# Kernel optimization log

Measured on AMD Instinct MI355X. Metric: run time of the kernel, lower is better.

## Reference

```python
import jax, jax.numpy as jnp
import numpy as np

B, N, D = 2, 2048, 768
H = 12
HD = D // H  # 64

def setup_inputs() -> dict:
    key = jax.random.key(0)
    ks = jax.random.split(key, 5)
    scale = 1.0 / np.sqrt(D)
    return {
        "x": jax.random.normal(ks[0], (B, N, D), dtype=jnp.float32),
        "W_kqv": jax.random.normal(ks[1], (H, 3 * HD, D), dtype=jnp.float32) * scale,
        "b_kqv": jax.random.normal(ks[2], (H, 3 * HD), dtype=jnp.float32) * 0.01,
        "W_proj": jax.random.normal(ks[3], (D, D), dtype=jnp.float32) * scale,
        "b_proj": jax.random.normal(ks[4], (D,), dtype=jnp.float32) * 0.01,
    }

def reference(x, W_kqv, b_kqv, W_proj, b_proj):
    # Per-head Linear: x @ W_h^T + b_h, all heads at once -> [B, H, N, 3*HD]
    kqv = jnp.einsum('bnd,hod->bhno', x, W_kqv) + b_kqv[None, :, None, :]
    k, q, v = jnp.split(kqv, 3, axis=-1)  # each [B, H, N, HD]
    # scores = q @ k^T / sqrt(head_dim)  (attention_scores(a=k, b=q))
    scores = jnp.einsum('bhqd,bhkd->bhqk', q, k) / jnp.sqrt(jnp.asarray(HD, x.dtype))
    # causal mask (tril): masked_fill with -inf where mask == 0
    causal = jnp.tril(jnp.ones((N, N), dtype=bool))
    scores = jnp.where(causal[None, None, :, :], scores, -jnp.inf)
    attn = jax.nn.softmax(scores, axis=-1)
    sa = jnp.einsum('bhqk,bhkd->bhqd', attn, v)  # [B, H, N, HD]
    # concat heads along feature dim (head order preserved)
    sa = sa.transpose(0, 2, 1, 3).reshape(B, N, D)
    # output projection
    return sa @ W_proj.T + b_proj
```

## Files before the change

### kernel.cpp

```cpp
#include <hip/hip_runtime.h>

#define BB 2
#define SEQ 2048
#define DIM 768
#define NH 12
#define HD 64

typedef _Float16 half8 __attribute__((ext_vector_type(8)));
typedef float floatx4 __attribute__((ext_vector_type(4)));

__device__ __forceinline__ void gl_lds16(const _Float16* g, _Float16* l) {
    __builtin_amdgcn_global_load_lds(
        (const __attribute__((address_space(1))) void*)g,
        (__attribute__((address_space(3))) void*)l, 16, 0, 0);
}

__global__ __launch_bounds__(256)
void cvt3(const float* __restrict__ s0, _Float16* __restrict__ d0, int nb0,
          const float* __restrict__ s1, _Float16* __restrict__ d1, int nb1,
          const float* __restrict__ s2, _Float16* __restrict__ d2) {
    int b = blockIdx.x;
    const float* s; _Float16* d;
    if (b < nb0)            { s = s0; d = d0; }
    else if (b < nb0 + nb1) { s = s1; d = d1; b -= nb0; }
    else                    { s = s2; d = d2; b -= nb0 + nb1; }
    const int i = (b * 256 + threadIdx.x) * 8;
    float4 a = *(const float4*)(s + i);
    float4 c = *(const float4*)(s + i + 4);
    half8 h;
    h[0] = (_Float16)a.x; h[1] = (_Float16)a.y; h[2] = (_Float16)a.z; h[3] = (_Float16)a.w;
    h[4] = (_Float16)c.x; h[5] = (_Float16)c.y; h[6] = (_Float16)c.z; h[7] = (_Float16)c.w;
    *(half8*)(d + i) = h;
}

#define GEMM_CORE(ATYPE_PTR, BTYPE_PTR)                                         \
    __shared__ _Float16 Asl[128 * 32];                                          \
    __shared__ _Float16 Bsl[128 * 32];                                          \
    const int t = threadIdx.x, w = t >> 6, lane = t & 63;                       \
    const int quad = lane >> 4, l15 = lane & 15;                                \
    const int wm = w >> 1, wn = w & 1;                                          \
    const int m0 = blockIdx.y * 128, c0 = blockIdx.x * 128;                     \
    const floatx4 z4 = {0.f, 0.f, 0.f, 0.f};                                    \
    floatx4 acc[4][4];                                                          \
    _Pragma("unroll") for (int i = 0; i < 4; ++i)                               \
        _Pragma("unroll") for (int j = 0; j < 4; ++j) acc[i][j] = z4;           \
    const _Float16* pA = ATYPE_PTR + (size_t)(m0 + w * 32 + l15) * DIM + quad * 8; \
    const _Float16* pB = BTYPE_PTR + (size_t)(c0 + w * 32 + l15) * DIM + quad * 8; \
    _Float16* ldsA0 = &Asl[(w * 2 + 0) * 512];                                  \
    _Float16* ldsA1 = &Asl[(w * 2 + 1) * 512];                                  \
    _Float16* ldsB0 = &Bsl[(w * 2 + 0) * 512];                                  \
    _Float16* ldsB1 = &Bsl[(w * 2 + 1) * 512];                                  \
    for (int k0 = 0; k0 < DIM; k0 += 32) {                                      \
        __syncthreads();                                                        \
        gl_lds16(pA + k0, ldsA0);                                               \
        gl_lds16(pA + k0 + 16 * DIM, ldsA1);                                    \
        gl_lds16(pB + k0, ldsB0);                                               \
        gl_lds16(pB + k0 + 16 * DIM, ldsB1);                                    \
        __syncthreads();                                                        \
        half8 af[4], bf[4];                                                     \
        _Pragma("unroll") for (int i = 0; i < 4; ++i)                           \
            af[i] = *(const half8*)&Asl[(wm * 4 + i) * 512 + lane * 8];         \
        _Pragma("unroll") for (int j = 0; j < 4; ++j)                           \
            bf[j] = *(const half8*)&Bsl[(wn * 4 + j) * 512 + lane * 8];         \
        _Pragma("unroll") for (int i = 0; i < 4; ++i)                           \
            _Pragma("unroll") for (int j = 0; j < 4; ++j)                       \
                acc[i][j] = __builtin_amdgcn_mfma_f32_16x16x32_f16(             \
                    af[i], bf[j], acc[i][j], 0, 0, 0);                          \
    }

__global__ __launch_bounds__(256)
void kqv_gemm2(const _Float16* __restrict__ xh, const _Float16* __restrict__ Wh,
               const float* __restrict__ bias, _Float16* __restrict__ kb,
               _Float16* __restrict__ qb, _Float16* __restrict__ vb) {
    GEMM_CORE(xh, Wh)
    #pragma unroll
    for (int j = 0; j < 4; ++j) {
        const int cbase = c0 + (wn * 4 + j) * 16;
        const int h = cbase / 192;
        const int rem = cbase - h * 192;
        const int part = rem >> 6;
        const int d = (rem & 63) + l15;
        _Float16* dst = (part == 0) ? kb : (part == 1 ? qb : vb);
        const float bv = bias[cbase + l15];
        #pragma unroll
        for (int i = 0; i < 4; ++i)
            #pragma unroll
            for (int r = 0; r < 4; ++r) {
                const int m = m0 + (wm * 4 + i) * 16 + quad * 4 + r;
                const int bidx = m >> 11, n = m & (SEQ - 1);
                dst[(((size_t)(bidx * NH + h) * SEQ + n) << 6) + d] =
                    (_Float16)(acc[i][j][r] + bv);
            }
    }
}

__global__ __launch_bounds__(256)
void proj_gemm2(const _Float16* __restrict__ A, const _Float16* __restrict__ Wh,
                const float* __restrict__ bias, float* __restrict__ out) {
    GEMM_CORE(A, Wh)
    #pragma unroll
    for (int j = 0; j < 4; ++j) {
        const int cbase = c0 + (wn * 4 + j) * 16;
        const float bv = bias[cbase + l15];
        #pragma unroll
        for (int i = 0; i < 4; ++i)
            #pragma unroll
            for (int r = 0; r < 4; ++r) {
                const int m = m0 + (wm * 4 + i) * 16 + quad * 4 + r;
                out[(size_t)m * DIM + cbase + l15] = acc[i][j][r] + bv;
            }
    }
}

__global__ __launch_bounds__(256)
void v_transpose(const _Float16* __restrict__ vb, _Float16* __restrict__ vbT) {
    __shared__ _Float16 T[64 * 72];
    const int t = threadIdx.x;
    const int s0 = blockIdx.x * 64;
    const size_t base = (size_t)blockIdx.y * (SEQ * HD);
    {
        const int s = t >> 2, doff = (t & 3) * 16;
        const _Float16* src = vb + base + (size_t)(s0 + s) * HD + doff;
        *(half8*)&T[s * 72 + doff]     = *(const half8*)src;
        *(half8*)&T[s * 72 + doff + 8] = *(const half8*)(src + 8);
    }
    __syncthreads();
    {
        const int d = t >> 2, soff = (t & 3) * 16;
        half8 o0, o1;
        #pragma unroll
        for (int k = 0; k < 8; ++k) o0[k] = T[(soff + k) * 72 + d];
        #pragma unroll
        for (int k = 0; k < 8; ++k) o1[k] = T[(soff + 8 + k) * 72 + d];
        _Float16* dst = vbT + base + (size_t)d * SEQ + s0 + soff;
        *(half8*)dst       = o0;
        *(half8*)(dst + 8) = o1;
    }
}

__global__ __launch_bounds__(256)
void attn_mfma(const _Float16* __restrict__ qb, const _Float16* __restrict__ kbuf,
               const _Float16* __restrict__ vbT, _Float16* __restrict__ sa) {
    __shared__ _Float16 Kl[2][64 * 64];
    __shared__ _Float16 Vl[2][64 * 64];
    __shared__ _Float16 Pl[4][16 * 72];
    const int qt = blockIdx.x, bh = blockIdx.y;
    const int t = threadIdx.x, w = t >> 6, lane = t & 63, quad = lane >> 4, l15 = lane & 15;
    const size_t base = (size_t)bh * (SEQ * HD);
    const int i0 = qt * 64 + w * 16;
    _Float16* Pw = Pl[w];
    const _Float16* Kg = kbuf + base;
    const _Float16* Vg = vbT + base;

    const int lr = lane >> 3, gg = lane & 7;
    const int gs = (gg ^ (lr & 7)) * 8;

    half8 aq[2];
    aq[0] = *(const half8*)(qb + base + (size_t)(i0 + l15) * HD + quad * 8);
    aq[1] = *(const half8*)(qb + base + (size_t)(i0 + l15) * HD + 32 + quad * 8);
    #pragma unroll
    for (int k = 0; k < 8; ++k) {
        aq[0][k] = aq[0][k] * (_Float16)0.125f;
        aq[1][k] = aq[1][k] * (_Float16)0.125f;
    }

    const floatx4 z4 = {0.f, 0.f, 0.f, 0.f};
    floatx4 O[4];
    #pragma unroll
    for (int dt = 0; dt < 4; ++dt) O[dt] = z4;
    float l_part[4] = {0.f, 0.f, 0.f, 0.f};

    #pragma unroll
    for (int p = 0; p < 2; ++p) {
        const int c = w * 2 + p, row = c * 8 + lr;
        gl_lds16(Kg + (size_t)row * HD + gs,  &Kl[0][c * 512]);
        gl_lds16(Vg + (size_t)row * SEQ + gs, &Vl[0][c * 512]);
    }

    const int swz = l15 & 7;

    for (int kt = 0; kt <= qt; ++kt) {
        const int buf = kt & 1;
        const int j0 = kt * 64;
        __syncthreads();

        if (kt < qt) {
            const _Float16* Kn = Kg + (size_t)(j0 + 64) * HD;
            const _Float16* Vn = Vg + (j0 + 64);
            #pragma unroll
            for (int p = 0; p < 2; ++p) {
                const int c = w * 2 + p, row = c * 8 + lr;
                gl_lds16(Kn + (size_t)row * HD + gs,  &Kl[buf ^ 1][c * 512]);
                gl_lds16(Vn + (size_t)row * SEQ + gs, &Vl[buf ^ 1][c * 512]);
            }
        }

        floatx4 S[4];
        #pragma unroll
        for (int nt = 0; nt < 4; ++nt) S[nt] = z4;
        #pragma unroll
        for (int ks = 0; ks < 2; ++ks)
            #pragma unroll
            for (int nt = 0; nt < 4; ++nt) {
                half8 bk = *(const half8*)&Kl[buf][(nt * 16 + l15) * 64 +
                                                   (((ks * 4 + quad) ^ swz) << 3)];
                S[nt] = __builtin_amdgcn_mfma_f32_16x16x32_f16(aq[ks], bk, S[nt], 0, 0, 0);
            }

        const bool diag = (kt == qt);
        asm volatile("" ::: "memory");
        #pragma unroll
        for (int nt = 0; nt < 4; ++nt) {
            const int j = j0 + nt * 16 + l15;
            #pragma unroll
            for (int r = 0; r < 4; ++r) {
                float p = __expf(S[nt][r]);
                if (diag && j > (i0 + quad * 4 + r)) p = 0.f;
                l_part[r] += p;
                Pw[(quad * 4 + r) * 72 + nt * 16 + l15] = (_Float16)p;
            }
        }
        asm volatile("" ::: "memory");
        #pragma unroll
        for (int ks = 0; ks < 2; ++ks) {
            half8 ap = *(const half8*)&Pw[l15 * 72 + ks * 32 + quad * 8];
            #pragma unroll
            for (int dt = 0; dt < 4; ++dt) {
                half8 bv = *(const half8*)&Vl[buf][(dt * 16 + l15) * 64 +
                                                    (((ks * 4 + quad) ^ swz) << 3)];
                O[dt] = __builtin_amdgcn_mfma_f32_16x16x32_f16(ap, bv, O[dt], 0, 0, 0);
            }
        }
    }

    const int bidx = bh / NH, h = bh - bidx * NH;
    #pragma unroll
    for (int r = 0; r < 4; ++r) {
        float rs = l_part[r];
        #pragma unroll
        for (int off = 1; off < 16; off <<= 1) rs += __shfl_xor(rs, off);
        const float inv = 1.0f / rs;
        const int i = i0 + quad * 4 + r;
        #pragma unroll
        for (int dt = 0; dt < 4; ++dt)
            sa[(size_t)(bidx * SEQ + i) * DIM + h * HD + dt * 16 + l15] =
                (_Float16)(O[dt][r] * inv);
    }
}

extern "C" void kernel_launch(void* const* d_in, const int* in_sizes, int n_in,
                              void* d_out, int out_size, void* d_ws, size_t ws_size,
                              hipStream_t stream) {
    (void)in_sizes; (void)n_in; (void)out_size; (void)ws_size;
    const float* x  = (const float*)d_in[0];
    const float* Wk = (const float*)d_in[1];
    const float* bk = (const float*)d_in[2];
    const float* Wp = (const float*)d_in[3];
    const float* bp = (const float*)d_in[4];
    float* out = (float*)d_out;

    _Float16* ws = (_Float16*)d_ws;
    const size_t per = (size_t)BB * NH * SEQ * HD;
    const int nx = BB * SEQ * DIM;
    const int nwk = NH * 3 * HD * DIM;
    const int nwp = DIM * DIM;
    _Float16* kb  = ws;
    _Float16* qb  = ws + per;
    _Float16* vb  = ws + 2 * per;
    _Float16* vbT = ws + 3 * per;
    _Float16* sa  = ws + 4 * per;
    _Float16* xh  = ws + 5 * per;
    _Float16* Wkh = xh + nx;
    _Float16* Wph = Wkh + nwk;

    const int nb0 = nx / 2048, nb1 = nwk / 2048, nb2 = nwp / 2048;
    cvt3<<<dim3(nb0 + nb1 + nb2), 256, 0, stream>>>(x, xh, nb0, Wk, Wkh, nb1, Wp, Wph);

    kqv_gemm2 <<<dim3(18, 32), 256, 0, stream>>>(xh, Wkh, bk, kb, qb, vb);
    v_transpose<<<dim3(32, 24), 256, 0, stream>>>(vb, vbT);
    attn_mfma <<<dim3(32, 24), 256, 0, stream>>>(qb, kb, vbT, sa);
    proj_gemm2<<<dim3(6, 32), 256, 0, stream>>>(sa, Wph, bp, out);
}
```

Baseline: 191.3 us.

## Double-buffer GEMM LDS tiles and widen attention query tile to 128 rows

The shared GEMM core now double-buffers its A/B tiles in LDS and prefetches the next K-slice before computing the current one, which removes one barrier per iteration and overlaps global loads with MFMA work. The attention kernel now gives each block 128 query rows (32 per wave, two row tiles), so every K/V tile loaded into LDS serves twice as many rows. Blocks are launched in reverse order so the longest causal blocks start first. In exchange there are half as many attention blocks (384), more registers per wave, waves that skip tiles fully above the diagonal while still joining the barriers, and more LDS use.

Result: slower. 215.2 us (+12.5%).

```diff
diff --git a/kernel.cpp b/kernel.cpp
--- a/kernel.cpp
+++ b/kernel.cpp
@@ -33,9 +33,9 @@
     *(half8*)(d + i) = h;
 }
 
-#define GEMM_CORE(ATYPE_PTR, BTYPE_PTR)                                         \
-    __shared__ _Float16 Asl[128 * 32];                                          \
-    __shared__ _Float16 Bsl[128 * 32];                                          \
+#define GEMM_CORE(APTR, BPTR)                                                   \
+    __shared__ _Float16 Asl[2][128 * 32];                                       \
+    __shared__ _Float16 Bsl[2][128 * 32];                                       \
     const int t = threadIdx.x, w = t >> 6, lane = t & 63;                       \
     const int quad = lane >> 4, l15 = lane & 15;                                \
     const int wm = w >> 1, wn = w & 1;                                          \
@@ -44,24 +44,26 @@
     floatx4 acc[4][4];                                                          \
     _Pragma("unroll") for (int i = 0; i < 4; ++i)                               \
         _Pragma("unroll") for (int j = 0; j < 4; ++j) acc[i][j] = z4;           \
-    const _Float16* pA = ATYPE_PTR + (size_t)(m0 + w * 32 + l15) * DIM + quad * 8; \
-    const _Float16* pB = BTYPE_PTR + (size_t)(c0 + w * 32 + l15) * DIM + quad * 8; \
-    _Float16* ldsA0 = &Asl[(w * 2 + 0) * 512];                                  \
-    _Float16* ldsA1 = &Asl[(w * 2 + 1) * 512];                                  \
-    _Float16* ldsB0 = &Bsl[(w * 2 + 0) * 512];                                  \
-    _Float16* ldsB1 = &Bsl[(w * 2 + 1) * 512];                                  \
-    for (int k0 = 0; k0 < DIM; k0 += 32) {                                      \
+    const _Float16* pA = APTR + (size_t)(m0 + w * 32 + l15) * DIM + quad * 8;   \
+    const _Float16* pB = BPTR + (size_t)(c0 + w * 32 + l15) * DIM + quad * 8;   \
+    gl_lds16(pA,            &Asl[0][(w * 2 + 0) * 512]);                        \
+    gl_lds16(pA + 16 * DIM, &Asl[0][(w * 2 + 1) * 512]);                        \
+    gl_lds16(pB,            &Bsl[0][(w * 2 + 0) * 512]);                        \
+    gl_lds16(pB + 16 * DIM, &Bsl[0][(w * 2 + 1) * 512]);                        \
+    for (int k0 = 0, it = 0; k0 < DIM; k0 += 32, ++it) {                        \
+        const int buf = it & 1;                                                 \
         __syncthreads();                                                        \
-        gl_lds16(pA + k0, ldsA0);                                               \
-        gl_lds16(pA + k0 + 16 * DIM, ldsA1);                                    \
-        gl_lds16(pB + k0, ldsB0);                                               \
-        gl_lds16(pB + k0 + 16 * DIM, ldsB1);                                    \
-        __syncthreads();                                                        \
+        if (k0 + 32 < DIM) {                                                    \
+            gl_lds16(pA + k0 + 32,            &Asl[buf ^ 1][(w * 2 + 0) * 512]);\
+            gl_lds16(pA + k0 + 32 + 16 * DIM, &Asl[buf ^ 1][(w * 2 + 1) * 512]);\
+            gl_lds16(pB + k0 + 32,            &Bsl[buf ^ 1][(w * 2 + 0) * 512]);\
+            gl_lds16(pB + k0 + 32 + 16 * DIM, &Bsl[buf ^ 1][(w * 2 + 1) * 512]);\
+        }                                                                       \
         half8 af[4], bf[4];                                                     \
         _Pragma("unroll") for (int i = 0; i < 4; ++i)                           \
-            af[i] = *(const half8*)&Asl[(wm * 4 + i) * 512 + lane * 8];         \
+            af[i] = *(const half8*)&Asl[buf][(wm * 4 + i) * 512 + lane * 8];    \
         _Pragma("unroll") for (int j = 0; j < 4; ++j)                           \
-            bf[j] = *(const half8*)&Bsl[(wn * 4 + j) * 512 + lane * 8];         \
+            bf[j] = *(const half8*)&Bsl[buf][(wn * 4 + j) * 512 + lane * 8];    \
         _Pragma("unroll") for (int i = 0; i < 4; ++i)                           \
             _Pragma("unroll") for (int j = 0; j < 4; ++j)                       \
                 acc[i][j] = __builtin_amdgcn_mfma_f32_16x16x32_f16(             \
@@ -143,32 +145,38 @@
                const _Float16* __restrict__ vbT, _Float16* __restrict__ sa) {
     __shared__ _Float16 Kl[2][64 * 64];
     __shared__ _Float16 Vl[2][64 * 64];
-    __shared__ _Float16 Pl[4][16 * 72];
-    const int qt = blockIdx.x, bh = blockIdx.y;
+    __shared__ _Float16 Pl[4][2][16 * 72];
+    const int Q = 15 - blockIdx.x;
+    const int bh = blockIdx.y;
     const int t = threadIdx.x, w = t >> 6, lane = t & 63, quad = lane >> 4, l15 = lane & 15;
     const size_t base = (size_t)bh * (SEQ * HD);
-    const int i0 = qt * 64 + w * 16;
-    _Float16* Pw = Pl[w];
+    const int i0 = Q * 128 + w * 32;
     const _Float16* Kg = kbuf + base;
     const _Float16* Vg = vbT + base;
+    const int nkt = 2 * Q + 2;
 
     const int lr = lane >> 3, gg = lane & 7;
     const int gs = (gg ^ (lr & 7)) * 8;
 
-    half8 aq[2];
-    aq[0] = *(const half8*)(qb + base + (size_t)(i0 + l15) * HD + quad * 8);
-    aq[1] = *(const half8*)(qb + base + (size_t)(i0 + l15) * HD + 32 + quad * 8);
-    #pragma unroll
-    for (int k = 0; k < 8; ++k) {
-        aq[0][k] = aq[0][k] * (_Float16)0.125f;
-        aq[1][k] = aq[1][k] * (_Float16)0.125f;
-    }
+    half8 aq[2][2];
+    #pragma unroll
+    for (int rt = 0; rt < 2; ++rt)
+        #pragma unroll
+        for (int ks = 0; ks < 2; ++ks) {
+            aq[rt][ks] = *(const half8*)(qb + base +
+                          (size_t)(i0 + rt * 16 + l15) * HD + ks * 32 + quad * 8);
+            #pragma unroll
+            for (int k = 0; k < 8; ++k)
+                aq[rt][ks][k] = aq[rt][ks][k] * (_Float16)0.125f;
+        }
 
     const floatx4 z4 = {0.f, 0.f, 0.f, 0.f};
-    floatx4 O[4];
-    #pragma unroll
-    for (int dt = 0; dt < 4; ++dt) O[dt] = z4;
-    float l_part[4] = {0.f, 0.f, 0.f, 0.f};
+    floatx4 O[2][4];
+    float l_part[2][4];
+    #pragma unroll
+    for (int rt = 0; rt < 2; ++rt)
+        #pragma unroll
+        for (int k = 0; k < 4; ++k) { O[rt][k] = z4; l_part[rt][k] = 0.f; }
 
     #pragma unroll
     for (int p = 0; p < 2; ++p) {
@@ -179,12 +187,12 @@
 
     const int swz = l15 & 7;
 
-    for (int kt = 0; kt <= qt; ++kt) {
+    for (int kt = 0; kt < nkt; ++kt) {
         const int buf = kt & 1;
         const int j0 = kt * 64;
         __syncthreads();
 
-        if (kt < qt) {
+        if (kt + 1 < nkt) {
             const _Float16* Kn = Kg + (size_t)(j0 + 64) * HD;
             const _Float16* Vn = Vg + (j0 + 64);
             #pragma unroll
@@ -194,58 +202,68 @@
                 gl_lds16(Vn + (size_t)row * SEQ + gs, &Vl[buf ^ 1][c * 512]);
             }
         }
-
-        floatx4 S[4];
-        #pragma unroll
-        for (int nt = 0; nt < 4; ++nt) S[nt] = z4;
+        if (j0 > i0 + 31) continue;
+
+        floatx4 S[2][4];
+        #pragma unroll
+        for (int rt = 0; rt < 2; ++rt)
+            #pragma unroll
+            for (int nt = 0; nt < 4; ++nt) S[rt][nt] = z4;
         #pragma unroll
         for (int ks = 0; ks < 2; ++ks)
             #pragma unroll
             for (int nt = 0; nt < 4; ++nt) {
                 half8 bk = *(const half8*)&Kl[buf][(nt * 16 + l15) * 64 +
                                                    (((ks * 4 + quad) ^ swz) << 3)];
-                S[nt] = __builtin_amdgcn_mfma_f32_16x16x32_f16(aq[ks], bk, S[nt], 0, 0, 0);
-            }
-
-        const bool diag = (kt == qt);
+                S[0][nt] = __builtin_amdgcn_mfma_f32_16x16x32_f16(aq[0][ks], bk, S[0][nt], 0, 0, 0);
+                S[1][nt] = __builtin_amdgcn_mfma_f32_16x16x32_f16(aq[1][ks], bk, S[1][nt], 0, 0, 0);
+            }
+
+        const bool needmask = (j0 + 63 > i0);
         asm volatile("" ::: "memory");
         #pragma unroll
-        for (int nt = 0; nt < 4; ++nt) {
-            const int j = j0 + nt * 16 + l15;
-            #pragma unroll
-            for (int r = 0; r < 4; ++r) {
-                float p = __expf(S[nt][r]);
-                if (diag && j > (i0 + quad * 4 + r)) p = 0.f;
-                l_part[r] += p;
-                Pw[(quad * 4 + r) * 72 + nt * 16 + l15] = (_Float16)p;
-            }
-        }
+        for (int rt = 0; rt < 2; ++rt)
+            #pragma unroll
+            for (int nt = 0; nt < 4; ++nt) {
+                const int j = j0 + nt * 16 + l15;
+                #pragma unroll
+                for (int r = 0; r < 4; ++r) {
+                    float p = __expf(S[rt][nt][r]);
+                    if (needmask && j > (i0 + rt * 16 + quad * 4 + r)) p = 0.f;
+                    l_part[rt][r] += p;
+                    Pl[w][rt][(quad * 4 + r) * 72 + nt * 16 + l15] = (_Float16)p;
+                }
+            }
         asm volatile("" ::: "memory");
         #pragma unroll
         for (int ks = 0; ks < 2; ++ks) {
-            half8 ap = *(const half8*)&Pw[l15 * 72 + ks * 32 + quad * 8];
+            half8 ap0 = *(const half8*)&Pl[w][0][l15 * 72 + ks * 32 + quad * 8];
+            half8 ap1 = *(const half8*)&Pl[w][1][l15 * 72 + ks * 32 + quad * 8];
             #pragma unroll
             for (int dt = 0; dt < 4; ++dt) {
                 half8 bv = *(const half8*)&Vl[buf][(dt * 16 + l15) * 64 +
                                                     (((ks * 4 + quad) ^ swz) << 3)];
-                O[dt] = __builtin_amdgcn_mfma_f32_16x16x32_f16(ap, bv, O[dt], 0, 0, 0);
+                O[0][dt] = __builtin_amdgcn_mfma_f32_16x16x32_f16(ap0, bv, O[0][dt], 0, 0, 0);
+                O[1][dt] = __builtin_amdgcn_mfma_f32_16x16x32_f16(ap1, bv, O[1][dt], 0, 0, 0);
             }
         }
     }
 
     const int bidx = bh / NH, h = bh - bidx * NH;
     #pragma unroll
-    for (int r = 0; r < 4; ++r) {
-        float rs = l_part[r];
-        #pragma unroll
-        for (int off = 1; off < 16; off <<= 1) rs += __shfl_xor(rs, off);
-        const float inv = 1.0f / rs;
-        const int i = i0 + quad * 4 + r;
-        #pragma unroll
-        for (int dt = 0; dt < 4; ++dt)
-            sa[(size_t)(bidx * SEQ + i) * DIM + h * HD + dt * 16 + l15] =
-                (_Float16)(O[dt][r] * inv);
-    }
+    for (int rt = 0; rt < 2; ++rt)
+        #pragma unroll
+        for (int r = 0; r < 4; ++r) {
+            float rs = l_part[rt][r];
+            #pragma unroll
+            for (int off = 1; off < 16; off <<= 1) rs += __shfl_xor(rs, off);
+            const float inv = 1.0f / rs;
+            const int i = i0 + rt * 16 + quad * 4 + r;
+            #pragma unroll
+            for (int dt = 0; dt < 4; ++dt)
+                sa[(size_t)(bidx * SEQ + i) * DIM + h * HD + dt * 16 + l15] =
+                    (_Float16)(O[rt][dt][r] * inv);
+        }
 }
 
 extern "C" void kernel_launch(void* const* d_in, const int* in_sizes, int n_in,
@@ -263,7 +281,6 @@
     const size_t per = (size_t)BB * NH * SEQ * HD;
     const int nx = BB * SEQ * DIM;
     const int nwk = NH * 3 * HD * DIM;
-    const int nwp = DIM * DIM;
     _Float16* kb  = ws;
     _Float16* qb  = ws + per;
     _Float16* vb  = ws + 2 * per;
@@ -273,11 +290,11 @@
     _Float16* Wkh = xh + nx;
     _Float16* Wph = Wkh + nwk;
 
-    const int nb0 = nx / 2048, nb1 = nwk / 2048, nb2 = nwp / 2048;
+    const int nb0 = nx / 2048, nb1 = nwk / 2048, nb2 = (DIM * DIM) / 2048;
     cvt3<<<dim3(nb0 + nb1 + nb2), 256, 0, stream>>>(x, xh, nb0, Wk, Wkh, nb1, Wp, Wph);
 
     kqv_gemm2 <<<dim3(18, 32), 256, 0, stream>>>(xh, Wkh, bk, kb, qb, vb);
     v_transpose<<<dim3(32, 24), 256, 0, stream>>>(vb, vbT);
-    attn_mfma <<<dim3(32, 24), 256, 0, stream>>>(qb, kb, vbT, sa);
+    attn_mfma <<<dim3(16, 24), 256, 0, stream>>>(qb, kb, vbT, sa);
     proj_gemm2<<<dim3(6, 32), 256, 0, stream>>>(sa, Wph, bp, out);
 }
```

## Split causal attention KV range across blocks and double-buffer GEMM LDS tiles

Applied to the files above, without the earlier changes.

Attention query tiles with long causal KV ranges are now split into up to four chunks of eight KV tiles, each handled by its own block. Partial unnormalized outputs and row sums go to workspace, and a new combine kernel sums them and normalizes. This removes the load imbalance where late query tiles dominate runtime, at the cost of an extra launch and extra global traffic for the partials. Separately, the shared GEMM core now double-buffers its LDS tiles so the next K slice loads while the current one is computed, and drops one barrier per iteration.

Result: no change. 188.9 us (-1.2%).

```diff
diff --git a/kernel.cpp b/kernel.cpp
--- a/kernel.cpp
+++ b/kernel.cpp
@@ -33,9 +33,9 @@
     *(half8*)(d + i) = h;
 }
 
-#define GEMM_CORE(ATYPE_PTR, BTYPE_PTR)                                         \
-    __shared__ _Float16 Asl[128 * 32];                                          \
-    __shared__ _Float16 Bsl[128 * 32];                                          \
+#define GEMM_CORE(APTR, BPTR)                                                   \
+    __shared__ _Float16 Asl[2][128 * 32];                                       \
+    __shared__ _Float16 Bsl[2][128 * 32];                                       \
     const int t = threadIdx.x, w = t >> 6, lane = t & 63;                       \
     const int quad = lane >> 4, l15 = lane & 15;                                \
     const int wm = w >> 1, wn = w & 1;                                          \
@@ -44,24 +44,26 @@
     floatx4 acc[4][4];                                                          \
     _Pragma("unroll") for (int i = 0; i < 4; ++i)                               \
         _Pragma("unroll") for (int j = 0; j < 4; ++j) acc[i][j] = z4;           \
-    const _Float16* pA = ATYPE_PTR + (size_t)(m0 + w * 32 + l15) * DIM + quad * 8; \
-    const _Float16* pB = BTYPE_PTR + (size_t)(c0 + w * 32 + l15) * DIM + quad * 8; \
-    _Float16* ldsA0 = &Asl[(w * 2 + 0) * 512];                                  \
-    _Float16* ldsA1 = &Asl[(w * 2 + 1) * 512];                                  \
-    _Float16* ldsB0 = &Bsl[(w * 2 + 0) * 512];                                  \
-    _Float16* ldsB1 = &Bsl[(w * 2 + 1) * 512];                                  \
-    for (int k0 = 0; k0 < DIM; k0 += 32) {                                      \
+    const _Float16* pA = APTR + (size_t)(m0 + w * 32 + l15) * DIM + quad * 8;   \
+    const _Float16* pB = BPTR + (size_t)(c0 + w * 32 + l15) * DIM + quad * 8;   \
+    gl_lds16(pA,            &Asl[0][(w * 2 + 0) * 512]);                        \
+    gl_lds16(pA + 16 * DIM, &Asl[0][(w * 2 + 1) * 512]);                        \
+    gl_lds16(pB,            &Bsl[0][(w * 2 + 0) * 512]);                        \
+    gl_lds16(pB + 16 * DIM, &Bsl[0][(w * 2 + 1) * 512]);                        \
+    for (int k0 = 0, it = 0; k0 < DIM; k0 += 32, ++it) {                        \
+        const int buf = it & 1;                                                 \
         __syncthreads();                                                        \
-        gl_lds16(pA + k0, ldsA0);                                               \
-        gl_lds16(pA + k0 + 16 * DIM, ldsA1);                                    \
-        gl_lds16(pB + k0, ldsB0);                                               \
-        gl_lds16(pB + k0 + 16 * DIM, ldsB1);                                    \
-        __syncthreads();                                                        \
+        if (k0 + 32 < DIM) {                                                    \
+            gl_lds16(pA + k0 + 32,            &Asl[buf ^ 1][(w * 2 + 0) * 512]);\
+            gl_lds16(pA + k0 + 32 + 16 * DIM, &Asl[buf ^ 1][(w * 2 + 1) * 512]);\
+            gl_lds16(pB + k0 + 32,            &Bsl[buf ^ 1][(w * 2 + 0) * 512]);\
+            gl_lds16(pB + k0 + 32 + 16 * DIM, &Bsl[buf ^ 1][(w * 2 + 1) * 512]);\
+        }                                                                       \
         half8 af[4], bf[4];                                                     \
         _Pragma("unroll") for (int i = 0; i < 4; ++i)                           \
-            af[i] = *(const half8*)&Asl[(wm * 4 + i) * 512 + lane * 8];         \
+            af[i] = *(const half8*)&Asl[buf][(wm * 4 + i) * 512 + lane * 8];    \
         _Pragma("unroll") for (int j = 0; j < 4; ++j)                           \
-            bf[j] = *(const half8*)&Bsl[(wn * 4 + j) * 512 + lane * 8];         \
+            bf[j] = *(const half8*)&Bsl[buf][(wn * 4 + j) * 512 + lane * 8];    \
         _Pragma("unroll") for (int i = 0; i < 4; ++i)                           \
             _Pragma("unroll") for (int j = 0; j < 4; ++j)                       \
                 acc[i][j] = __builtin_amdgcn_mfma_f32_16x16x32_f16(             \
@@ -140,11 +142,20 @@
 
 __global__ __launch_bounds__(256)
 void attn_mfma(const _Float16* __restrict__ qb, const _Float16* __restrict__ kbuf,
-               const _Float16* __restrict__ vbT, _Float16* __restrict__ sa) {
+               const _Float16* __restrict__ vbT, _Float16* __restrict__ sa,
+               _Float16* __restrict__ Opart, float* __restrict__ lpart) {
     __shared__ _Float16 Kl[2][64 * 64];
     __shared__ _Float16 Vl[2][64 * 64];
     __shared__ _Float16 Pl[4][16 * 72];
-    const int qt = blockIdx.x, bh = blockIdx.y;
+    int u = blockIdx.x, qt, p, np;
+    if (u < 8)       { qt = u;                            p = 0;      np = 1; }
+    else if (u < 24) { int v = u - 8;  qt = 8  + (v >> 1); p = v & 1; np = 2; }
+    else if (u < 48) { int v = u - 24; qt = 16 + v / 3;    p = v % 3; np = 3; }
+    else             { int v = u - 48; qt = 24 + (v >> 2); p = v & 3; np = 4; }
+    const int kt0 = p * 8;
+    const int ktn = (p == np - 1) ? (qt - kt0 + 1) : 8;
+
+    const int bh = blockIdx.y;
     const int t = threadIdx.x, w = t >> 6, lane = t & 63, quad = lane >> 4, l15 = lane & 15;
     const size_t base = (size_t)bh * (SEQ * HD);
     const int i0 = qt * 64 + w * 16;
@@ -171,25 +182,26 @@
     float l_part[4] = {0.f, 0.f, 0.f, 0.f};
 
     #pragma unroll
-    for (int p = 0; p < 2; ++p) {
-        const int c = w * 2 + p, row = c * 8 + lr;
-        gl_lds16(Kg + (size_t)row * HD + gs,  &Kl[0][c * 512]);
-        gl_lds16(Vg + (size_t)row * SEQ + gs, &Vl[0][c * 512]);
+    for (int pp = 0; pp < 2; ++pp) {
+        const int c = w * 2 + pp, row = c * 8 + lr;
+        gl_lds16(Kg + (size_t)(kt0 * 64 + row) * HD + gs,  &Kl[0][c * 512]);
+        gl_lds16(Vg + (size_t)row * SEQ + kt0 * 64 + gs,   &Vl[0][c * 512]);
     }
 
     const int swz = l15 & 7;
 
-    for (int kt = 0; kt <= qt; ++kt) {
-        const int buf = kt & 1;
+    for (int it = 0; it < ktn; ++it) {
+        const int kt = kt0 + it;
+        const int buf = it & 1;
         const int j0 = kt * 64;
         __syncthreads();
 
-        if (kt < qt) {
+        if (it + 1 < ktn) {
             const _Float16* Kn = Kg + (size_t)(j0 + 64) * HD;
             const _Float16* Vn = Vg + (j0 + 64);
             #pragma unroll
-            for (int p = 0; p < 2; ++p) {
-                const int c = w * 2 + p, row = c * 8 + lr;
+            for (int pp = 0; pp < 2; ++pp) {
+                const int c = w * 2 + pp, row = c * 8 + lr;
                 gl_lds16(Kn + (size_t)row * HD + gs,  &Kl[buf ^ 1][c * 512]);
                 gl_lds16(Vn + (size_t)row * SEQ + gs, &Vl[buf ^ 1][c * 512]);
             }
@@ -214,10 +226,10 @@
             const int j = j0 + nt * 16 + l15;
             #pragma unroll
             for (int r = 0; r < 4; ++r) {
-                float p = __expf(S[nt][r]);
-                if (diag && j > (i0 + quad * 4 + r)) p = 0.f;
-                l_part[r] += p;
-                Pw[(quad * 4 + r) * 72 + nt * 16 + l15] = (_Float16)p;
+                float pv = __expf(S[nt][r]);
+                if (diag && j > (i0 + quad * 4 + r)) pv = 0.f;
+                l_part[r] += pv;
+                Pw[(quad * 4 + r) * 72 + nt * 16 + l15] = (_Float16)pv;
             }
         }
         asm volatile("" ::: "memory");
@@ -233,19 +245,69 @@
         }
     }
 
+    if (np == 1) {
+        const int bidx = bh / NH, h = bh - bidx * NH;
+        #pragma unroll
+        for (int r = 0; r < 4; ++r) {
+            float rs = l_part[r];
+            #pragma unroll
+            for (int off = 1; off < 16; off <<= 1) rs += __shfl_xor(rs, off);
+            const float inv = 1.0f / rs;
+            const int i = i0 + quad * 4 + r;
+            #pragma unroll
+            for (int dt = 0; dt < 4; ++dt)
+                sa[(size_t)(bidx * SEQ + i) * DIM + h * HD + dt * 16 + l15] =
+                    (_Float16)(O[dt][r] * inv);
+        }
+    } else {
+        const size_t slot = ((size_t)(bh * 32 + qt) * 4 + p);
+        _Float16* Od = Opart + slot * 4096;
+        float*    ld = lpart + slot * 64;
+        #pragma unroll
+        for (int r = 0; r < 4; ++r) {
+            float rs = l_part[r];
+            #pragma unroll
+            for (int off = 1; off < 16; off <<= 1) rs += __shfl_xor(rs, off);
+            const int row = w * 16 + quad * 4 + r;
+            ld[row] = rs;
+            #pragma unroll
+            for (int dt = 0; dt < 4; ++dt)
+                Od[row * 64 + dt * 16 + l15] = (_Float16)O[dt][r];
+        }
+    }
+}
+
+__global__ __launch_bounds__(256)
+void attn_combine(const _Float16* __restrict__ Opart, const float* __restrict__ lpart,
+                  _Float16* __restrict__ sa) {
+    const int qt = 8 + blockIdx.x;
+    const int bh = blockIdx.y;
+    const int np = (qt >> 3) + 1;
+    const int t = threadIdx.x;
+    const int row = t >> 2, d0 = (t & 3) * 16;
+    const size_t slot0 = ((size_t)(bh * 32 + qt) * 4);
+
+    float lsum = 0.f;
+    for (int p = 0; p < np; ++p) lsum += lpart[(slot0 + p) * 64 + row];
+
+    float acc[16];
+    #pragma unroll
+    for (int k = 0; k < 16; ++k) acc[k] = 0.f;
+    for (int p = 0; p < np; ++p) {
+        const _Float16* src = Opart + (slot0 + p) * 4096 + row * 64 + d0;
+        half8 a = *(const half8*)src;
+        half8 b = *(const half8*)(src + 8);
+        #pragma unroll
+        for (int k = 0; k < 8; ++k) { acc[k] += (float)a[k]; acc[8 + k] += (float)b[k]; }
+    }
+    const float inv = 1.0f / lsum;
     const int bidx = bh / NH, h = bh - bidx * NH;
-    #pragma unroll
-    for (int r = 0; r < 4; ++r) {
-        float rs = l_part[r];
-        #pragma unroll
-        for (int off = 1; off < 16; off <<= 1) rs += __shfl_xor(rs, off);
-        const float inv = 1.0f / rs;
-        const int i = i0 + quad * 4 + r;
-        #pragma unroll
-        for (int dt = 0; dt < 4; ++dt)
-            sa[(size_t)(bidx * SEQ + i) * DIM + h * HD + dt * 16 + l15] =
-                (_Float16)(O[dt][r] * inv);
-    }
+    _Float16* dst = sa + (size_t)(bidx * SEQ + qt * 64 + row) * DIM + h * HD + d0;
+    half8 o0, o1;
+    #pragma unroll
+    for (int k = 0; k < 8; ++k) { o0[k] = (_Float16)(acc[k] * inv); o1[k] = (_Float16)(acc[8 + k] * inv); }
+    *(half8*)dst       = o0;
+    *(half8*)(dst + 8) = o1;
 }
 
 extern "C" void kernel_launch(void* const* d_in, const int* in_sizes, int n_in,
@@ -272,12 +334,15 @@
     _Float16* xh  = ws + 5 * per;
     _Float16* Wkh = xh + nx;
     _Float16* Wph = Wkh + nwk;
+    _Float16* Opart = Wph + nwp;
+    float*    lpart = (float*)(Opart + (size_t)24 * 32 * 4 * 4096);
 
     const int nb0 = nx / 2048, nb1 = nwk / 2048, nb2 = nwp / 2048;
     cvt3<<<dim3(nb0 + nb1 + nb2), 256, 0, stream>>>(x, xh, nb0, Wk, Wkh, nb1, Wp, Wph);
 
-    kqv_gemm2 <<<dim3(18, 32), 256, 0, stream>>>(xh, Wkh, bk, kb, qb, vb);
+    kqv_gemm2  <<<dim3(18, 32), 256, 0, stream>>>(xh, Wkh, bk, kb, qb, vb);
     v_transpose<<<dim3(32, 24), 256, 0, stream>>>(vb, vbT);
-    attn_mfma <<<dim3(32, 24), 256, 0, stream>>>(qb, kb, vbT, sa);
-    proj_gemm2<<<dim3(6, 32), 256, 0, stream>>>(sa, Wph, bp, out);
-}
+    attn_mfma  <<<dim3(80, 24), 256, 0, stream>>>(qb, kb, vbT, sa, Opart, lpart);
+    attn_combine<<<dim3(24, 24), 256, 0, stream>>>(Opart, lpart, sa);
+    proj_gemm2 <<<dim3(6, 32), 256, 0, stream>>>(sa, Wph, bp, out);
+}
```
